# Performance work log

Hardware: AMD Instinct MI355X
Metric: run time of the kernel (lower is better)

The kernel has to match this reference:

```python
import jax, jax.numpy as jnp
import numpy as np

CELL = 14
NC = 80
BPC = 3
IMG = 448.0
CS = IMG / CELL  # cell pixel size
CLASS_SCALE = 1.0
OBJECT_SCALE = 1.0
NOOBJECT_SCALE = 0.5
COORD_SCALE = 5.0
EPS = 1e-9

# base_boxes[y, x, b, :] = (x*CS, y*CS, 0, 0)
_gy, _gx = jnp.meshgrid(jnp.arange(CELL, dtype=jnp.float32), jnp.arange(CELL, dtype=jnp.float32), indexing='ij')
BASE = jnp.broadcast_to(jnp.stack([_gx * CS, _gy * CS, jnp.zeros_like(_gx), jnp.zeros_like(_gx)], axis=-1)[:, :, None, :], (CELL, CELL, BPC, 4))
MULT = jnp.array([CS, CS, IMG, IMG], dtype=jnp.float32)


def _ciou(boxes1, box2):
    # boxes1: [S,S,BPC,4] (cx,cy,w,h); box2: [4]
    b1_cx, b1_cy, b1_w, b1_h = boxes1[..., 0], boxes1[..., 1], boxes1[..., 2], boxes1[..., 3]
    b2_cx, b2_cy, b2_w, b2_h = box2[0], box2[1], box2[2], box2[3]
    b1_x1, b1_y1, b1_x2, b1_y2 = b1_cx - b1_w / 2, b1_cy - b1_h / 2, b1_cx + b1_w / 2, b1_cy + b1_h / 2
    b2_x1, b2_y1, b2_x2, b2_y2 = b2_cx - b2_w / 2, b2_cy - b2_h / 2, b2_cx + b2_w / 2, b2_cy + b2_h / 2
    inter = jnp.clip(jnp.minimum(b1_x2, b2_x2) - jnp.maximum(b1_x1, b2_x1), 0) * \
            jnp.clip(jnp.minimum(b1_y2, b2_y2) - jnp.maximum(b1_y1, b2_y1), 0)
    union = b1_w * b1_h + b2_w * b2_h - inter
    iou = inter / (union + EPS)
    center_distance = (b1_cx - b2_cx) ** 2 + (b1_cy - b2_cy) ** 2
    # faithful to original (uses center/size components for the enclosing box)
    enclose_left = jnp.minimum(boxes1[..., 0], box2[0])
    enclose_right = jnp.maximum(boxes1[..., 2], box2[2])
    enclose_top = jnp.minimum(boxes1[..., 1], box2[1])
    enclose_bottom = jnp.maximum(boxes1[..., 3], box2[3])
    enclose_diag = (enclose_right - enclose_left) ** 2 + (enclose_bottom - enclose_top) ** 2
    v = (4.0 / jnp.pi ** 2) * (jnp.arctan(b2_w / (b2_h + EPS)) - jnp.arctan(b1_w / (b1_h + EPS))) ** 2
    alpha = jax.lax.stop_gradient(v / (1 - iou + v + EPS))
    return iou - center_distance / (enclose_diag + EPS) - alpha * v  # [S,S,BPC]


def _l2(t):
    return 0.5 * jnp.sum(t * t)


def _per_object_loss(predict, label):
    # predict: [S,S,NC+5*BPC], label: [5]
    gy = jnp.arange(CELL, dtype=jnp.float32)[:, None]
    gx = jnp.arange(CELL, dtype=jnp.float32)[None, :]
    x, y, w, h = label[0], label[1], label[2], label[3]
    min_x = jnp.floor((x - w / 2) / CS)
    max_x = jnp.minimum(jnp.ceil((x + w / 2) / CS), CELL)
    min_y = jnp.floor((y - h / 2) / CS)
    max_y = jnp.minimum(jnp.ceil((y + h / 2) / CS), CELL)
    object_mask = ((gx >= min_x) & (gx < max_x) & (gy >= min_y) & (gy < max_y)).astype(jnp.float32)
    cx, cy = jnp.floor(x / CS), jnp.floor(y / CS)
    center_mask = ((gx == cx) & (gy == cy)).astype(jnp.float32)

    pboxes = predict[:, :, NC + BPC:].reshape(CELL, CELL, BPC, 4) * MULT + BASE
    iou = _ciou(pboxes, label[:4])                     # [S,S,BPC]
    C = iou * center_mask[..., None]
    I = (iou >= jnp.max(iou, axis=-1, keepdims=True)).astype(jnp.float32) * center_mask[..., None]
    no_I = 1.0 - I
    p_C = predict[:, :, NC:NC + BPC]

    sqrt_w, sqrt_h = jnp.sqrt(jnp.abs(w)), jnp.sqrt(jnp.abs(h))
    p_x, p_y = pboxes[..., 0], pboxes[..., 1]
    p_sqrt_w = jnp.sqrt(jnp.clip(pboxes[..., 2], 0.0, IMG))
    p_sqrt_h = jnp.sqrt(jnp.clip(pboxes[..., 3], 0.0, IMG))

    P = jax.nn.one_hot(label[4].astype(jnp.int32), NC, dtype=jnp.float32)
    p_P = predict[:, :, :NC]

    class_loss = _l2(object_mask[..., None] * (p_P - P)) * CLASS_SCALE
    object_loss = _l2(I * (p_C - C)) * OBJECT_SCALE
    noobject_loss = _l2(no_I * p_C) * NOOBJECT_SCALE
    coord_loss = (_l2(I * (p_x - x) / CS) + _l2(I * (p_y - y) / CS)
                  + _l2(I * (p_sqrt_w - sqrt_w)) / IMG + _l2(I * (p_sqrt_h - sqrt_h)) / IMG) * COORD_SCALE
    return class_loss + object_loss + noobject_loss + coord_loss


def setup_inputs() -> dict:
    key = jax.random.key(0)
    k1, k2, k3, k4, k5 = jax.random.split(key, 5)
    B, M = 1024, 30
    predicts = jax.random.normal(k1, (B, CELL, CELL, NC + 5 * BPC), dtype=jnp.float32) * 0.1
    xy = jax.random.uniform(k2, (B, M, 2), minval=60.0, maxval=IMG - 60.0)
    wh = jax.random.uniform(k3, (B, M, 2), minval=10.0, maxval=100.0)
    cls = jax.random.randint(k4, (B, M, 1), 0, NC).astype(jnp.float32)
    labels = jnp.concatenate([xy, wh, cls], axis=-1)
    objects_num = jax.random.randint(k5, (B,), 1, M + 1).astype(jnp.int32)
    return {"predicts": predicts, "labels": labels, "objects_num": objects_num}


def reference(predicts, labels, objects_num):
    B, M = labels.shape[0], labels.shape[1]
    per_batch = jax.vmap(lambda p, ls: jax.vmap(lambda l: _per_object_loss(p, l))(ls))
    losses = per_batch(predicts, labels)  # [B, M]
    mask = (jnp.arange(M)[None, :] < objects_num[:, None]).astype(jnp.float32)
    return jnp.sum(losses * mask) / B
```

## Files before the change

### kernel.cpp

```cpp
#include <hip/hip_runtime.h>
#include <math.h>

#define CELLN 14
#define NCELLS 196
#define NCLS 80
#define NCH 95
#define NDW (NCELLS * NCH)
#define NF4 (NDW / 4)
#define NW32 (NCELLS * 20)

__global__ __launch_bounds__(256) void yolo_loss_kernel(
    const float* __restrict__ predicts,
    const float* __restrict__ labels,
    const int* __restrict__ objects_num,
    float* __restrict__ out,
    int M, float invB)
{
    __shared__ unsigned s_W32[NW32];
    __shared__ float    s_cnt[NCELLS];
    __shared__ float    s_red[4];

    const int img  = blockIdx.x;
    const int tid  = threadIdx.x;
    const int lane = tid & 63;
    const int wid  = tid >> 6;
    const float inv32 = 1.0f / 32.0f;

    const float*  gpred = predicts + (size_t)img * NDW;
    const float4* gp4   = (const float4*)gpred;
    const int n = objects_num[img];

    for (int i = tid; i < NW32; i += 256) s_W32[i] = 0u;
    for (int i = tid; i < NCELLS; i += 256) s_cnt[i] = 0.0f;
    __syncthreads();

    float acc = 0.0f;
    for (int g = (tid >> 3); g < n; g += 32) {
        const int r = tid & 7;
        const float* lab = labels + ((size_t)img * M + g) * 5;
        const float x = lab[0], y = lab[1], w = lab[2], h = lab[3];
        const int cls = (int)lab[4];

        int min_x = max(0, (int)floorf((x - w * 0.5f) * inv32));
        int max_x = min(CELLN, (int)ceilf((x + w * 0.5f) * inv32));
        int min_y = max(0, (int)floorf((y - h * 0.5f) * inv32));
        int max_y = min(CELLN, (int)ceilf((y + h * 0.5f) * inv32));
        int nx = max_x - min_x;
        int ncell = nx * (max_y - min_y);

        if (r == 0) acc += 0.5f * (float)ncell;
        const unsigned winc = 1u << (8 * (cls & 3));
        const int      woff = cls >> 2;
        for (int p = r; p < ncell; p += 8) {
            int cell = (min_y + p / nx) * CELLN + (min_x + p % nx);
            atomicAdd(&s_cnt[cell], 1.0f);
            atomicAdd(&s_W32[cell * 20 + woff], winc);
        }
    }
    __syncthreads();

    float pc2 = 0.0f;
    #pragma unroll
    for (int i = 0; i < 19; ++i) {
        int f = tid + (i << 8);
        if (f < NF4) {
            float4 v4 = gp4[f];
            unsigned idx  = (unsigned)f << 2;
            unsigned cell = idx / 95u;
            unsigned ch   = idx - cell * 95u;
            float vv[4] = {v4.x, v4.y, v4.z, v4.w};
            #pragma unroll
            for (int k = 0; k < 4; ++k) {
                float v = vv[k];
                if (ch < (unsigned)NCLS) {
                    unsigned wword = s_W32[cell * 20 + (ch >> 2)];
                    float wgt = (float)((wword >> (8 * (ch & 3))) & 255u);
                    acc += 0.5f * s_cnt[cell] * v * v - wgt * v;
                } else if (ch < 83u) {
                    pc2 += v * v;
                }
                ++ch;
                if (ch == 95u) { ch = 0u; ++cell; }
            }
        }
    }
    acc += 0.25f * (float)n * pc2;

    for (int o = tid; o < n; o += 256) {
        const float* lab = labels + ((size_t)img * M + o) * 5;
        const float x = lab[0], y = lab[1], w = lab[2], h = lab[3];

        int cx = (int)floorf(x * inv32);
        int cy = (int)floorf(y * inv32);
        const float* cp = gpred + (cy * CELLN + cx) * NCH;
        float bx = (float)cx * 32.0f;
        float by = (float)cy * 32.0f;

        float pC[3], ciou[3], pxv[3], pyv[3], pwv[3], phv[3];
        #pragma unroll
        for (int b = 0; b < 3; ++b) {
            pC[b] = cp[NCLS + b];
            float px = cp[83 + 4*b] * 32.0f + bx;
            float py = cp[84 + 4*b] * 32.0f + by;
            float pw = cp[85 + 4*b] * 448.0f;
            float ph = cp[86 + 4*b] * 448.0f;
            pxv[b] = px; pyv[b] = py; pwv[b] = pw; phv[b] = ph;
            float iw = fminf(px + pw*0.5f, x + w*0.5f) - fmaxf(px - pw*0.5f, x - w*0.5f);
            float ih = fminf(py + ph*0.5f, y + h*0.5f) - fmaxf(py - ph*0.5f, y - h*0.5f);
            iw = fmaxf(iw, 0.0f); ih = fmaxf(ih, 0.0f);
            float inter = iw * ih;
            float uni = pw*ph + w*h - inter;
            float iou = inter / (uni + 1e-9f);
            float cd = (px - x)*(px - x) + (py - y)*(py - y);
            float el = fminf(px, x), er = fmaxf(pw, w);
            float et = fminf(py, y), eb = fmaxf(ph, h);
            float ed = (er - el)*(er - el) + (eb - et)*(eb - et);
            float da = atanf(w / (h + 1e-9f)) - atanf(pw / (ph + 1e-9f));
            float v = 0.40528473456935108577f * da * da;
            float alpha = v / (1.0f - iou + v + 1e-9f);
            ciou[b] = iou - cd / (ed + 1e-9f) - alpha * v;
        }
        float mx = fmaxf(ciou[0], fmaxf(ciou[1], ciou[2]));
        float sqw = sqrtf(fabsf(w)), sqh = sqrtf(fabsf(h));
        float sel_obj = 0.0f, sel_pc2 = 0.0f, coord = 0.0f;
        #pragma unroll
        for (int b = 0; b < 3; ++b) {
            if (ciou[b] >= mx) {
                float d = pC[b] - ciou[b];
                sel_obj += d * d;
                sel_pc2 += pC[b] * pC[b];
                float dx = (pxv[b] - x) * inv32;
                float dy = (pyv[b] - y) * inv32;
                float psw = sqrtf(fminf(fmaxf(pwv[b], 0.0f), 448.0f));
                float psh = sqrtf(fminf(fmaxf(phv[b], 0.0f), 448.0f));
                float dw = psw - sqw, dh = psh - sqh;
                coord += dx*dx + dy*dy + (dw*dw + dh*dh) * (1.0f/448.0f);
            }
        }
        acc += 0.5f * sel_obj - 0.25f * sel_pc2 + 2.5f * coord;
    }

    #pragma unroll
    for (int off = 32; off; off >>= 1) acc += __shfl_down(acc, off);
    if (lane == 0) s_red[wid] = acc;
    __syncthreads();
    if (tid == 0) {
        atomicAdd(out, (s_red[0] + s_red[1] + s_red[2] + s_red[3]) * invB);
    }
}

extern "C" void kernel_launch(void* const* d_in, const int* in_sizes, int n_in,
                              void* d_out, int out_size, void* d_ws, size_t ws_size,
                              hipStream_t stream) {
    const float* predicts = (const float*)d_in[0];
    const float* labels   = (const float*)d_in[1];
    const int*   objn     = (const int*)d_in[2];
    float* out = (float*)d_out;

    const int B = in_sizes[2];
    const int M = in_sizes[1] / (B * 5);

    yolo_loss_kernel<<<dim3(B), dim3(256), 0, stream>>>(
        predicts, labels, objn, out, M, 1.0f / (float)B);
}
```

Baseline: 119.5 us.

## Split each image across four blocks and batch prediction loads upfront

Launches four blocks per image, each streaming a quarter of the prediction tensor, with all of its float4 loads issued into registers before the compute loop. The goal is more blocks in flight and more memory-level parallelism on a bandwidth-bound reduction. The cost is that every block rebuilds the per-image class/count shared tables, which is redundant work, and there are four times as many global atomics on the output. Object and per-box work now runs only in part 0. The label loop assumes n <= 32, so objects past 32 would be dropped if M exceeded 32.

```diff
diff --git a/kernel.cpp b/kernel.cpp
--- a/kernel.cpp
+++ b/kernel.cpp
@@ -8,6 +8,8 @@
 #define NDW (NCELLS * NCH)
 #define NF4 (NDW / 4)
 #define NW32 (NCELLS * 20)
+#define SPLIT 4
+#define CHUNK ((NF4 + SPLIT - 1) / SPLIT)
 
 __global__ __launch_bounds__(256) void yolo_loss_kernel(
     const float* __restrict__ predicts,
@@ -20,7 +22,8 @@
     __shared__ float    s_cnt[NCELLS];
     __shared__ float    s_red[4];
 
-    const int img  = blockIdx.x;
+    const int img  = blockIdx.x >> 2;
+    const int part = blockIdx.x & 3;
     const int tid  = threadIdx.x;
     const int lane = tid & 63;
     const int wid  = tid >> 6;
@@ -35,36 +38,50 @@
     __syncthreads();
 
     float acc = 0.0f;
-    for (int g = (tid >> 3); g < n; g += 32) {
+    {
+        const int g = tid >> 3;
         const int r = tid & 7;
-        const float* lab = labels + ((size_t)img * M + g) * 5;
-        const float x = lab[0], y = lab[1], w = lab[2], h = lab[3];
-        const int cls = (int)lab[4];
+        if (g < n) {
+            const float* lab = labels + ((size_t)img * M + g) * 5;
+            const float x = lab[0], y = lab[1], w = lab[2], h = lab[3];
+            const int cls = (int)lab[4];
 
-        int min_x = max(0, (int)floorf((x - w * 0.5f) * inv32));
-        int max_x = min(CELLN, (int)ceilf((x + w * 0.5f) * inv32));
-        int min_y = max(0, (int)floorf((y - h * 0.5f) * inv32));
-        int max_y = min(CELLN, (int)ceilf((y + h * 0.5f) * inv32));
-        int nx = max_x - min_x;
-        int ncell = nx * (max_y - min_y);
+            int min_x = max(0, (int)floorf((x - w * 0.5f) * inv32));
+            int max_x = min(CELLN, (int)ceilf((x + w * 0.5f) * inv32));
+            int min_y = max(0, (int)floorf((y - h * 0.5f) * inv32));
+            int max_y = min(CELLN, (int)ceilf((y + h * 0.5f) * inv32));
+            int nx = max_x - min_x;
+            int ncell = nx * (max_y - min_y);
 
-        if (r == 0) acc += 0.5f * (float)ncell;
-        const unsigned winc = 1u << (8 * (cls & 3));
-        const int      woff = cls >> 2;
-        for (int p = r; p < ncell; p += 8) {
-            int cell = (min_y + p / nx) * CELLN + (min_x + p % nx);
-            atomicAdd(&s_cnt[cell], 1.0f);
-            atomicAdd(&s_W32[cell * 20 + woff], winc);
+            if (r == 0 && part == 0) acc += 0.5f * (float)ncell;
+            const unsigned winc = 1u << (8 * (cls & 3));
+            const int      woff = cls >> 2;
+            for (int p = r; p < ncell; p += 8) {
+                int cell = (min_y + p / nx) * CELLN + (min_x + p % nx);
+                atomicAdd(&s_cnt[cell], 1.0f);
+                atomicAdd(&s_W32[cell * 20 + woff], winc);
+            }
         }
     }
     __syncthreads();
 
+    const int f_lo = part * CHUNK;
+    const int f_hi = min(NF4, f_lo + CHUNK);
+    const int f0   = f_lo + tid;
+
+    float4 vals[5];
+    #pragma unroll
+    for (int j = 0; j < 5; ++j) {
+        int f = f0 + (j << 8);
+        if (f < f_hi) vals[j] = gp4[f];
+    }
+
     float pc2 = 0.0f;
     #pragma unroll
-    for (int i = 0; i < 19; ++i) {
-        int f = tid + (i << 8);
-        if (f < NF4) {
-            float4 v4 = gp4[f];
+    for (int j = 0; j < 5; ++j) {
+        int f = f0 + (j << 8);
+        if (f < f_hi) {
+            float4 v4 = vals[j];
             unsigned idx  = (unsigned)f << 2;
             unsigned cell = idx / 95u;
             unsigned ch   = idx - cell * 95u;
@@ -75,7 +92,7 @@
                 if (ch < (unsigned)NCLS) {
                     unsigned wword = s_W32[cell * 20 + (ch >> 2)];
                     float wgt = (float)((wword >> (8 * (ch & 3))) & 255u);
-                    acc += 0.5f * s_cnt[cell] * v * v - wgt * v;
+                    acc += v * (0.5f * s_cnt[cell] * v - wgt);
                 } else if (ch < 83u) {
                     pc2 += v * v;
                 }
@@ -86,58 +103,60 @@
     }
     acc += 0.25f * (float)n * pc2;
 
-    for (int o = tid; o < n; o += 256) {
-        const float* lab = labels + ((size_t)img * M + o) * 5;
-        const float x = lab[0], y = lab[1], w = lab[2], h = lab[3];
+    if (part == 0) {
+        for (int o = tid; o < n; o += 256) {
+            const float* lab = labels + ((size_t)img * M + o) * 5;
+            const float x = lab[0], y = lab[1], w = lab[2], h = lab[3];
 
-        int cx = (int)floorf(x * inv32);
-        int cy = (int)floorf(y * inv32);
-        const float* cp = gpred + (cy * CELLN + cx) * NCH;
-        float bx = (float)cx * 32.0f;
-        float by = (float)cy * 32.0f;
+            int cx = (int)floorf(x * inv32);
+            int cy = (int)floorf(y * inv32);
+            const float* cp = gpred + (cy * CELLN + cx) * NCH;
+            float bx = (float)cx * 32.0f;
+            float by = (float)cy * 32.0f;
 
-        float pC[3], ciou[3], pxv[3], pyv[3], pwv[3], phv[3];
-        #pragma unroll
-        for (int b = 0; b < 3; ++b) {
-            pC[b] = cp[NCLS + b];
-            float px = cp[83 + 4*b] * 32.0f + bx;
-            float py = cp[84 + 4*b] * 32.0f + by;
-            float pw = cp[85 + 4*b] * 448.0f;
-            float ph = cp[86 + 4*b] * 448.0f;
-            pxv[b] = px; pyv[b] = py; pwv[b] = pw; phv[b] = ph;
-            float iw = fminf(px + pw*0.5f, x + w*0.5f) - fmaxf(px - pw*0.5f, x - w*0.5f);
-            float ih = fminf(py + ph*0.5f, y + h*0.5f) - fmaxf(py - ph*0.5f, y - h*0.5f);
-            iw = fmaxf(iw, 0.0f); ih = fmaxf(ih, 0.0f);
-            float inter = iw * ih;
-            float uni = pw*ph + w*h - inter;
-            float iou = inter / (uni + 1e-9f);
-            float cd = (px - x)*(px - x) + (py - y)*(py - y);
-            float el = fminf(px, x), er = fmaxf(pw, w);
-            float et = fminf(py, y), eb = fmaxf(ph, h);
-            float ed = (er - el)*(er - el) + (eb - et)*(eb - et);
-            float da = atanf(w / (h + 1e-9f)) - atanf(pw / (ph + 1e-9f));
-            float v = 0.40528473456935108577f * da * da;
-            float alpha = v / (1.0f - iou + v + 1e-9f);
-            ciou[b] = iou - cd / (ed + 1e-9f) - alpha * v;
+            float pC[3], ciou[3], pxv[3], pyv[3], pwv[3], phv[3];
+            #pragma unroll
+            for (int b = 0; b < 3; ++b) {
+                pC[b] = cp[NCLS + b];
+                float px = cp[83 + 4*b] * 32.0f + bx;
+                float py = cp[84 + 4*b] * 32.0f + by;
+                float pw = cp[85 + 4*b] * 448.0f;
+                float ph = cp[86 + 4*b] * 448.0f;
+                pxv[b] = px; pyv[b] = py; pwv[b] = pw; phv[b] = ph;
+                float iw = fminf(px + pw*0.5f, x + w*0.5f) - fmaxf(px - pw*0.5f, x - w*0.5f);
+                float ih = fminf(py + ph*0.5f, y + h*0.5f) - fmaxf(py - ph*0.5f, y - h*0.5f);
+                iw = fmaxf(iw, 0.0f); ih = fmaxf(ih, 0.0f);
+                float inter = iw * ih;
+                float uni = pw*ph + w*h - inter;
+                float iou = inter / (uni + 1e-9f);
+                float cd = (px - x)*(px - x) + (py - y)*(py - y);
+                float el = fminf(px, x), er = fmaxf(pw, w);
+                float et = fminf(py, y), eb = fmaxf(ph, h);
+                float ed = (er - el)*(er - el) + (eb - et)*(eb - et);
+                float da = atanf(w / (h + 1e-9f)) - atanf(pw / (ph + 1e-9f));
+                float v = 0.40528473456935108577f * da * da;
+                float alpha = v / (1.0f - iou + v + 1e-9f);
+                ciou[b] = iou - cd / (ed + 1e-9f) - alpha * v;
+            }
+            float mx = fmaxf(ciou[0], fmaxf(ciou[1], ciou[2]));
+            float sqw = sqrtf(fabsf(w)), sqh = sqrtf(fabsf(h));
+            float sel_obj = 0.0f, sel_pc2 = 0.0f, coord = 0.0f;
+            #pragma unroll
+            for (int b = 0; b < 3; ++b) {
+                if (ciou[b] >= mx) {
+                    float d = pC[b] - ciou[b];
+                    sel_obj += d * d;
+                    sel_pc2 += pC[b] * pC[b];
+                    float dx = (pxv[b] - x) * inv32;
+                    float dy = (pyv[b] - y) * inv32;
+                    float psw = sqrtf(fminf(fmaxf(pwv[b], 0.0f), 448.0f));
+                    float psh = sqrtf(fminf(fmaxf(phv[b], 0.0f), 448.0f));
+                    float dw = psw - sqw, dh = psh - sqh;
+                    coord += dx*dx + dy*dy + (dw*dw + dh*dh) * (1.0f/448.0f);
+                }
+            }
+            acc += 0.5f * sel_obj - 0.25f * sel_pc2 + 2.5f * coord;
         }
-        float mx = fmaxf(ciou[0], fmaxf(ciou[1], ciou[2]));
-        float sqw = sqrtf(fabsf(w)), sqh = sqrtf(fabsf(h));
-        float sel_obj = 0.0f, sel_pc2 = 0.0f, coord = 0.0f;
-        #pragma unroll
-        for (int b = 0; b < 3; ++b) {
-            if (ciou[b] >= mx) {
-                float d = pC[b] - ciou[b];
-                sel_obj += d * d;
-                sel_pc2 += pC[b] * pC[b];
-                float dx = (pxv[b] - x) * inv32;
-                float dy = (pyv[b] - y) * inv32;
-                float psw = sqrtf(fminf(fmaxf(pwv[b], 0.0f), 448.0f));
-                float psh = sqrtf(fminf(fmaxf(phv[b], 0.0f), 448.0f));
-                float dw = psw - sqw, dh = psh - sqh;
-                coord += dx*dx + dy*dy + (dw*dw + dh*dh) * (1.0f/448.0f);
-            }
-        }
-        acc += 0.5f * sel_obj - 0.25f * sel_pc2 + 2.5f * coord;
     }
 
     #pragma unroll
@@ -160,6 +179,6 @@
     const int B = in_sizes[2];
     const int M = in_sizes[1] / (B * 5);
 
-    yolo_loss_kernel<<<dim3(B), dim3(256), 0, stream>>>(
+    yolo_loss_kernel<<<dim3(B * SPLIT), dim3(256), 0, stream>>>(
         predicts, labels, objn, out, M, 1.0f / (float)B);
 }
```

Result: slower. 148.1 us (+23.9%).

## Precompute per-cell sums of squares in a separate pass and gather per object

Applied to the files above, without the earlier changes.

The class loss is expanded algebraically. Each covered cell contributes its sum of squared class logits, minus twice the logit of the label's class, plus one. A new first kernel computes per-cell sums of squared class and confidence values into workspace using 16-lane shuffle reductions. The per-image kernel then gathers only the cells each object covers, which removes the shared-memory atomic histograms and the weighted full-image pass. The cost is an extra launch and a workspace round trip, and the object loop now handles at most 32 objects per image.

```diff
diff --git a/kernel.cpp b/kernel.cpp
--- a/kernel.cpp
+++ b/kernel.cpp
@@ -6,85 +6,102 @@
 #define NCLS 80
 #define NCH 95
 #define NDW (NCELLS * NCH)
-#define NF4 (NDW / 4)
-#define NW32 (NCELLS * 20)
 
-__global__ __launch_bounds__(256) void yolo_loss_kernel(
+__global__ __launch_bounds__(256, 8) void yolo_ss_kernel(
+    const float* __restrict__ predicts,
+    float* __restrict__ ss_cls,
+    float* __restrict__ ss_conf,
+    int total_cells)
+{
+    const int tid = threadIdx.x;
+    const int sub = tid & 15;
+    const int cluster = blockIdx.x * 16 + (tid >> 4);
+    const int g0 = cluster * 2;
+    const int g1 = g0 + 1;
+    const bool ok0 = g0 < total_cells;
+    const bool ok1 = g1 < total_cells;
+    const float* b0 = predicts + (size_t)g0 * NCH;
+    const float* b1 = predicts + (size_t)g1 * NCH;
+
+    float v[12];
+    #pragma unroll
+    for (int j = 0; j < 5; ++j) v[j]     = ok0 ? b0[j * 16 + sub] : 0.0f;
+    v[5]  = (ok0 && sub < 3) ? b0[NCLS + sub] : 0.0f;
+    #pragma unroll
+    for (int j = 0; j < 5; ++j) v[6 + j] = ok1 ? b1[j * 16 + sub] : 0.0f;
+    v[11] = (ok1 && sub < 3) ? b1[NCLS + sub] : 0.0f;
+
+    float a0 = 0.0f, a1 = 0.0f;
+    #pragma unroll
+    for (int j = 0; j < 5; ++j) { a0 += v[j] * v[j]; a1 += v[6 + j] * v[6 + j]; }
+    float c0 = v[5] * v[5], c1 = v[11] * v[11];
+
+    #pragma unroll
+    for (int m = 8; m; m >>= 1) {
+        a0 += __shfl_xor(a0, m, 16);
+        a1 += __shfl_xor(a1, m, 16);
+        c0 += __shfl_xor(c0, m, 16);
+        c1 += __shfl_xor(c1, m, 16);
+    }
+    if (sub == 0) {
+        if (ok0) { ss_cls[g0] = a0; ss_conf[g0] = c0; }
+        if (ok1) { ss_cls[g1] = a1; ss_conf[g1] = c1; }
+    }
+}
+
+__global__ __launch_bounds__(256) void yolo_obj_kernel(
     const float* __restrict__ predicts,
     const float* __restrict__ labels,
     const int* __restrict__ objects_num,
+    const float* __restrict__ ss_cls,
+    const float* __restrict__ ss_conf,
     float* __restrict__ out,
     int M, float invB)
 {
-    __shared__ unsigned s_W32[NW32];
-    __shared__ float    s_cnt[NCELLS];
-    __shared__ float    s_red[4];
-
+    __shared__ float s_red[4];
     const int img  = blockIdx.x;
     const int tid  = threadIdx.x;
     const int lane = tid & 63;
     const int wid  = tid >> 6;
     const float inv32 = 1.0f / 32.0f;
 
-    const float*  gpred = predicts + (size_t)img * NDW;
-    const float4* gp4   = (const float4*)gpred;
+    const float* gpred = predicts + (size_t)img * NDW;
     const int n = objects_num[img];
 
-    for (int i = tid; i < NW32; i += 256) s_W32[i] = 0u;
-    for (int i = tid; i < NCELLS; i += 256) s_cnt[i] = 0.0f;
+    float sc = (tid < NCELLS) ? ss_conf[img * NCELLS + tid] : 0.0f;
+    #pragma unroll
+    for (int off = 32; off; off >>= 1) sc += __shfl_down(sc, off);
+    if (lane == 0) s_red[wid] = sc;
     __syncthreads();
+    const float S_pC2 = s_red[0] + s_red[1] + s_red[2] + s_red[3];
 
     float acc = 0.0f;
-    for (int g = (tid >> 3); g < n; g += 32) {
+    if (tid == 0) acc = 0.25f * (float)n * S_pC2;
+
+    {
+        const int g = tid >> 3;
         const int r = tid & 7;
-        const float* lab = labels + ((size_t)img * M + g) * 5;
-        const float x = lab[0], y = lab[1], w = lab[2], h = lab[3];
-        const int cls = (int)lab[4];
+        if (g < n) {
+            const float* lab = labels + ((size_t)img * M + g) * 5;
+            const float x = lab[0], y = lab[1], w = lab[2], h = lab[3];
+            const int cls = (int)lab[4];
 
-        int min_x = max(0, (int)floorf((x - w * 0.5f) * inv32));
-        int max_x = min(CELLN, (int)ceilf((x + w * 0.5f) * inv32));
-        int min_y = max(0, (int)floorf((y - h * 0.5f) * inv32));
-        int max_y = min(CELLN, (int)ceilf((y + h * 0.5f) * inv32));
-        int nx = max_x - min_x;
-        int ncell = nx * (max_y - min_y);
+            int min_x = max(0, (int)floorf((x - w * 0.5f) * inv32));
+            int max_x = min(CELLN, (int)ceilf((x + w * 0.5f) * inv32));
+            int min_y = max(0, (int)floorf((y - h * 0.5f) * inv32));
+            int max_y = min(CELLN, (int)ceilf((y + h * 0.5f) * inv32));
+            int nx = max_x - min_x;
+            int ncell = nx * (max_y - min_y);
 
-        if (r == 0) acc += 0.5f * (float)ncell;
-        const unsigned winc = 1u << (8 * (cls & 3));
-        const int      woff = cls >> 2;
-        for (int p = r; p < ncell; p += 8) {
-            int cell = (min_y + p / nx) * CELLN + (min_x + p % nx);
-            atomicAdd(&s_cnt[cell], 1.0f);
-            atomicAdd(&s_W32[cell * 20 + woff], winc);
+            float csum = 0.0f;
+            for (int p = r; p < ncell; p += 8) {
+                int cell  = (min_y + p / nx) * CELLN + (min_x + p % nx);
+                int gcell = img * NCELLS + cell;
+                csum += ss_cls[gcell] - 2.0f * predicts[(size_t)gcell * NCH + cls] + 1.0f;
+            }
+            acc += 0.5f * csum;
         }
     }
-    __syncthreads();
-
-    float pc2 = 0.0f;
-    #pragma unroll
-    for (int i = 0; i < 19; ++i) {
-        int f = tid + (i << 8);
-        if (f < NF4) {
-            float4 v4 = gp4[f];
-            unsigned idx  = (unsigned)f << 2;
-            unsigned cell = idx / 95u;
-            unsigned ch   = idx - cell * 95u;
-            float vv[4] = {v4.x, v4.y, v4.z, v4.w};
-            #pragma unroll
-            for (int k = 0; k < 4; ++k) {
-                float v = vv[k];
-                if (ch < (unsigned)NCLS) {
-                    unsigned wword = s_W32[cell * 20 + (ch >> 2)];
-                    float wgt = (float)((wword >> (8 * (ch & 3))) & 255u);
-                    acc += 0.5f * s_cnt[cell] * v * v - wgt * v;
-                } else if (ch < 83u) {
-                    pc2 += v * v;
-                }
-                ++ch;
-                if (ch == 95u) { ch = 0u; ++cell; }
-            }
-        }
-    }
-    acc += 0.25f * (float)n * pc2;
 
     for (int o = tid; o < n; o += 256) {
         const float* lab = labels + ((size_t)img * M + o) * 5;
@@ -142,6 +159,7 @@
 
     #pragma unroll
     for (int off = 32; off; off >>= 1) acc += __shfl_down(acc, off);
+    __syncthreads();
     if (lane == 0) s_red[wid] = acc;
     __syncthreads();
     if (tid == 0) {
@@ -160,6 +178,14 @@
     const int B = in_sizes[2];
     const int M = in_sizes[1] / (B * 5);
 
-    yolo_loss_kernel<<<dim3(B), dim3(256), 0, stream>>>(
-        predicts, labels, objn, out, M, 1.0f / (float)B);
+    const int total_cells = B * NCELLS;
+    float* ss_cls  = (float*)d_ws;
+    float* ss_conf = ss_cls + total_cells;
+
+    const int blocksA = (total_cells + 31) / 32;
+    yolo_ss_kernel<<<dim3(blocksA), dim3(256), 0, stream>>>(
+        predicts, ss_cls, ss_conf, total_cells);
+
+    yolo_obj_kernel<<<dim3(B), dim3(256), 0, stream>>>(
+        predicts, labels, objn, ss_cls, ss_conf, out, M, 1.0f / (float)B);
 }
```

After: 123.7 us. 3.5% more time.
